# Optimization experiments

Hardware: AMD Instinct MI355X
Metric: run time of the kernel (lower is better)

## Reference

```python
import jax, jax.numpy as jnp
import numpy as np

B, S, D, H, L = 128, 200, 512, 512, 2  # batch, seq(=max_seq_len), input, hidden, layers


def _uni(key, shape, fan):
    bound = 1.0 / np.sqrt(fan)
    return jax.random.uniform(key, shape, jnp.float32, -bound, bound)


def setup_inputs() -> dict:
    key = jax.random.key(0)
    ks = jax.random.split(key, 12)
    x = jax.random.normal(ks[0], (B, S, D), jnp.float32)
    lens = jax.random.randint(ks[1], (B,), 1, S + 1).astype(jnp.int64)
    return {
        'x': x,
        'lens': lens,
        'Wih_f': _uni(ks[2], (L, 4 * H, D), H),
        'Whh_f': _uni(ks[3], (L, 4 * H, H), H),
        'bih_f': _uni(ks[4], (L, 4 * H), H),
        'bhh_f': _uni(ks[5], (L, 4 * H), H),
        'Wih_b': _uni(ks[6], (L, 4 * H, D), H),
        'Whh_b': _uni(ks[7], (L, 4 * H, H), H),
        'bih_b': _uni(ks[8], (L, 4 * H), H),
        'bhh_b': _uni(ks[9], (L, 4 * H), H),
    }


def _lstm_dir(xs, Wih, Whh, bih, bhh, reverse):
    # xs: [B,S,Din]. Precompute batched input projection, scan the recurrence.
    gx = jnp.einsum('bsd,gd->bsg', xs, Wih) + bih  # [B,S,4H]
    h0 = jnp.zeros((xs.shape[0], Whh.shape[1]), xs.dtype)
    c0 = jnp.zeros_like(h0)

    def step(carry, g_t):
        h, c = carry
        gates = g_t + h @ Whh.T + bhh
        i, f, g, o = jnp.split(gates, 4, axis=-1)  # PyTorch LSTMCell order
        i = jax.nn.sigmoid(i)
        f = jax.nn.sigmoid(f)
        g = jnp.tanh(g)
        o = jax.nn.sigmoid(o)
        c = f * c + i * g
        h = o * jnp.tanh(c)
        return (h, c), h

    _, hs = jax.lax.scan(step, (h0, c0), jnp.swapaxes(gx, 0, 1), reverse=reverse)
    return jnp.swapaxes(hs, 0, 1)  # [B,S,H], time-ordered


def reference(x, lens, Wih_f, Whh_f, bih_f, bhh_f, Wih_b, Whh_b, bih_b, bhh_b):
    valid = (jnp.arange(S)[None, :] < lens[:, None]).astype(x.dtype)[..., None]  # [B,S,1]
    f_in, b_in = x, x
    for l in range(L):
        f_h = _lstm_dir(f_in, Wih_f[l], Whh_f[l], bih_f[l], bhh_f[l], reverse=False)
        b_h = _lstm_dir(b_in, Wih_b[l], Whh_b[l], bih_b[l], bhh_b[l], reverse=True)
        f_h = f_h * valid  # masked_fill(mask, 0) for positions >= lens
        b_h = b_h * valid
        f_in, b_in = f_h, b_h
    return jnp.concatenate((f_in, b_in), axis=2)  # [B,S,2H]
```

## Files before the change

kernel.cpp:

```cpp
#include <hip/hip_runtime.h>
#include <hip/hip_bf16.h>

typedef __bf16 bf16x8 __attribute__((ext_vector_type(8)));
typedef _Float16 f16x8 __attribute__((ext_vector_type(8)));
typedef float f32x4 __attribute__((ext_vector_type(4)));

__device__ __forceinline__ unsigned short f2bf(float f) {
    unsigned int u = __builtin_bit_cast(unsigned int, f);
    u += 0x7FFFu + ((u >> 16) & 1u);
    return (unsigned short)(u >> 16);
}
__device__ __forceinline__ float bf2f(unsigned short s) {
    unsigned int u = ((unsigned int)s) << 16;
    return __builtin_bit_cast(float, u);
}

__device__ __forceinline__ void ldg_c(uint4& d, const void* p) {
    asm volatile("global_load_dwordx4 %0, %1, off sc0 sc1" : "=v"(d) : "v"(p));
}
__device__ __forceinline__ void vm_drain() {
    asm volatile("s_waitcnt vmcnt(0)" ::: "memory");
    __builtin_amdgcn_sched_barrier(0);
}
__device__ __forceinline__ void lds_fence() {
    asm volatile("s_waitcnt lgkmcnt(0)" ::: "memory");
    __builtin_amdgcn_sched_barrier(0);
}
__device__ __forceinline__ void stg_c16(void* p, unsigned short v) {
    asm volatile("global_store_short %0, %1, off sc0 sc1" :: "v"(p), "v"(v) : "memory");
}

__device__ __forceinline__ void wait_flags(const unsigned* f, unsigned tgt) {
    int lane = threadIdx.x & 63;
    for (;;) {
        unsigned v = __hip_atomic_load(f + lane, __ATOMIC_RELAXED, __HIP_MEMORY_SCOPE_AGENT);
        if (__all((int)(v >= tgt))) break;
        __builtin_amdgcn_s_sleep(1);
    }
}

__global__ void prep_x(const float* __restrict__ x,
                       unsigned short* __restrict__ xh,
                       unsigned short* __restrict__ xl) {
    int g = blockIdx.x * 256 + threadIdx.x;
    if (g >= 1638400) return;
    int lane = g & 63;
    int kc   = (g >> 6) & 15;
    int nt   = (g >> 10) & 7;
    int t    = g >> 13;
    int batch = nt * 16 + (lane & 15);
    int k = kc * 32 + (lane >> 4) * 8;
    const float* s = x + ((size_t)batch * 200 + t) * 512 + k;
    float4 v0 = *(const float4*)s;
    float4 v1 = *(const float4*)(s + 4);
    float vv[8] = {v0.x, v0.y, v0.z, v0.w, v1.x, v1.y, v1.z, v1.w};
    unsigned int ph[4], pl[4];
    #pragma unroll
    for (int j = 0; j < 4; ++j) {
        float a = vv[2*j], b = vv[2*j+1];
        unsigned short ha = f2bf(a), hb = f2bf(b);
        unsigned short la = f2bf(a - bf2f(ha)), lb = f2bf(b - bf2f(hb));
        ph[j] = (unsigned)ha | ((unsigned)hb << 16);
        pl[j] = (unsigned)la | ((unsigned)lb << 16);
    }
    ((uint4*)xh)[g] = make_uint4(ph[0], ph[1], ph[2], ph[3]);
    ((uint4*)xl)[g] = make_uint4(pl[0], pl[1], pl[2], pl[3]);
}

__global__ void prep_w(const float* __restrict__ W,
                       unsigned short* __restrict__ wprep,
                       int dir, int isHH) {
    int g = blockIdx.x * 256 + threadIdx.x;
    if (g >= 262144) return;
    int lane = g & 63;
    int kc   = (g >> 6) & 15;
    int mt   = (g >> 10) & 1;
    int cu   = (g >> 11) & 63;
    int l    = g >> 17;
    int r = lane & 15;
    int grow = (2 * mt + (r >> 3)) * 512 + cu * 8 + (r & 7);
    int k = kc * 32 + (lane >> 4) * 8;
    const float* s = W + ((size_t)l * 2048 + grow) * 512 + k;
    float4 v0 = *(const float4*)s;
    float4 v1 = *(const float4*)(s + 4);
    float vv[8] = {v0.x, v0.y, v0.z, v0.w, v1.x, v1.y, v1.z, v1.w};
    bool f16fmt = isHH || (l == 1);
    unsigned int ph[4], pl[4];
    #pragma unroll
    for (int j = 0; j < 4; ++j) {
        float a = vv[2*j], b = vv[2*j+1];
        unsigned short ha, hb, la, lb;
        if (f16fmt) {
            _Float16 fa = (_Float16)a, fb = (_Float16)b;
            _Float16 ra = (_Float16)(a - (float)fa), rb = (_Float16)(b - (float)fb);
            ha = __builtin_bit_cast(unsigned short, fa);
            hb = __builtin_bit_cast(unsigned short, fb);
            la = __builtin_bit_cast(unsigned short, ra);
            lb = __builtin_bit_cast(unsigned short, rb);
        } else {
            ha = f2bf(a); hb = f2bf(b);
            la = f2bf(a - bf2f(ha)); lb = f2bf(b - bf2f(hb));
        }
        ph[j] = (unsigned)ha | ((unsigned)hb << 16);
        pl[j] = (unsigned)la | ((unsigned)lb << 16);
    }
    size_t blk = ((size_t)(dir * 2 + l) * 64 + cu) * 8192;
    size_t fH = blk + (size_t)((isHH * 2 + 0) * 2048 + mt * 1024 + kc * 64 + lane);
    size_t fL = blk + (size_t)((isHH * 2 + 1) * 2048 + mt * 1024 + kc * 64 + lane);
    ((uint4*)wprep)[fH] = make_uint4(ph[0], ph[1], ph[2], ph[3]);
    ((uint4*)wprep)[fL] = make_uint4(pl[0], pl[1], pl[2], pl[3]);
}

__global__ void bsum_k(const float* __restrict__ bih_f, const float* __restrict__ bhh_f,
                       const float* __restrict__ bih_b, const float* __restrict__ bhh_b,
                       float* __restrict__ bsum) {
    int i = blockIdx.x * 256 + threadIdx.x;
    if (i < 8192) {
        int dir = i >> 12, rem = i & 4095;
        const float* bi = dir ? bih_b : bih_f;
        const float* bh = dir ? bhh_b : bhh_f;
        bsum[i] = bi[rem] + bh[rem];
    }
}

__global__ void reset_k(uint4* __restrict__ p) {
    int g = blockIdx.x * 256 + threadIdx.x;
    if (g < 131136) p[g] = make_uint4(0, 0, 0, 0);
}

__global__ void __launch_bounds__(512)
lstm_persist(const unsigned short* __restrict__ xh,
             const unsigned short* __restrict__ xl,
             const unsigned short* __restrict__ wprep,
             const float*          __restrict__ bsum,
             unsigned short*       __restrict__ hbuf,
             const int*            __restrict__ lens,
             float*                __restrict__ dout,
             unsigned*             __restrict__ flagv)
{
    extern __shared__ char smem[];
    float* wexch = (float*)(smem + 131072);
    float* cst   = (float*)(smem + 131072 + 17408);

    const int bid  = blockIdx.x;
    const int xcd  = bid & 7;
    const int unit = xcd >> 1;
    const int slot = unit >> 1, dir = unit & 1;
    const int cu8  = ((xcd & 1) << 5) | (bid >> 3);
    const int hj0  = cu8 * 8;
    const int tid  = threadIdx.x;
    const int lane = tid & 63, ng = tid >> 6;
    const int l15  = lane & 15, kg = lane >> 4;
    const int wsel = dir * 2 + slot;

    const int sib = slot ? dir : (2 + dir);
    unsigned* own_f = flagv + unit * 64;
    unsigned* sib_f = flagv + sib * 64;

    {
        const uint4* src = (const uint4*)wprep + ((size_t)(wsel * 64 + cu8) * 8192);
        uint4* dst = (uint4*)smem;
        #pragma unroll
        for (int i = 0; i < 16; ++i) dst[tid + i * 512] = src[tid + i * 512];
    }
    for (int i = tid; i < 8 * 132; i += 512) cst[i] = 0.f;
    __syncthreads();

    const int lenv = lens[ng * 16 + l15];
    const int u    = lane >> 3;
    const int b2   = 2 * (lane & 7);
    const int gbA  = ng * 16 + b2, gbB = gbA + 1;
    const int lenA = lens[gbA], lenB = lens[gbB];
    const int hj   = hj0 + u;
    float bias_c[4];
    #pragma unroll
    for (int q = 0; q < 4; ++q) bias_c[q] = bsum[wsel * 2048 + q * 512 + hj];
    float* wex = wexch + ng * 32 * 17;
    const size_t lofs = (size_t)lane * 8;

    for (int tau = 0; tau <= 200; ++tau) {
        const int t = slot ? (tau - 1) : tau;
        const bool active = (t >= 0 && t <= 199);
        int t_eff = 0, p_w = 0, p_r = 0;
        if (active) { t_eff = dir ? (199 - t) : t; p_w = t & 3; p_r = (t + 3) & 3; }

        f32x4 acc0 = {0.f, 0.f, 0.f, 0.f};
        f32x4 acc1 = {0.f, 0.f, 0.f, 0.f};

        if (slot == 0 && active) {
            const unsigned short* XH = xh + (size_t)t_eff * 65536;
            const unsigned short* XL = xl + (size_t)t_eff * 65536;
            #pragma unroll
            for (int kc = 0; kc < 16; ++kc) {
                size_t bo = (size_t)ng * 8192 + (size_t)kc * 512 + lofs;
                bf16x8 bxh = *(const bf16x8*)(XH + bo);
                bf16x8 bxl = *(const bf16x8*)(XL + bo);
                const char* ab = smem + kc * 1024 + lane * 16;
                bf16x8 aih0 = *(const bf16x8*)(ab);
                bf16x8 ail0 = *(const bf16x8*)(ab + 32768);
                bf16x8 aih1 = *(const bf16x8*)(ab + 16384);
                bf16x8 ail1 = *(const bf16x8*)(ab + 16384 + 32768);
                acc0 = __builtin_amdgcn_mfma_f32_16x16x32_bf16(aih0, bxh, acc0, 0, 0, 0);
                acc0 = __builtin_amdgcn_mfma_f32_16x16x32_bf16(aih0, bxl, acc0, 0, 0, 0);
                acc0 = __builtin_amdgcn_mfma_f32_16x16x32_bf16(ail0, bxh, acc0, 0, 0, 0);
                acc1 = __builtin_amdgcn_mfma_f32_16x16x32_bf16(aih1, bxh, acc1, 0, 0, 0);
                acc1 = __builtin_amdgcn_mfma_f32_16x16x32_bf16(aih1, bxl, acc1, 0, 0, 0);
                acc1 = __builtin_amdgcn_mfma_f32_16x16x32_bf16(ail1, bxh, acc1, 0, 0, 0);
            }
        }

        {
            unsigned tgt = (unsigned)tau;
            if (ng == 0) wait_flags(own_f, tgt);
            if (slot == 1) { if (ng == 1) wait_flags(sib_f, tgt); }
            else if (tau >= 3) { if (ng == 1) wait_flags(sib_f, tgt - 2); }
        }
        __syncthreads();

        if (active) {
            const unsigned short* HH = hbuf + ((size_t)((slot * 4 + p_r) * 2 + dir) << 16);

            if (slot == 0) {
                uint4 vh[16];
                #pragma unroll
                for (int kc = 0; kc < 16; ++kc)
                    ldg_c(vh[kc], HH + (size_t)ng * 8192 + (size_t)kc * 512 + lofs);
                vm_drain();
                #pragma unroll
                for (int kc = 0; kc < 16; ++kc) {
                    f16x8 bh = __builtin_bit_cast(f16x8, vh[kc]);
                    const char* ab = smem + kc * 1024 + lane * 16;
                    f16x8 ahh0 = *(const f16x8*)(ab + 65536);
                    f16x8 ahl0 = *(const f16x8*)(ab + 98304);
                    f16x8 ahh1 = *(const f16x8*)(ab + 16384 + 65536);
                    f16x8 ahl1 = *(const f16x8*)(ab + 16384 + 98304);
                    acc0 = __builtin_amdgcn_mfma_f32_16x16x32_f16(ahh0, bh, acc0, 0, 0, 0);
                    acc0 = __builtin_amdgcn_mfma_f32_16x16x32_f16(ahl0, bh, acc0, 0, 0, 0);
                    acc1 = __builtin_amdgcn_mfma_f32_16x16x32_f16(ahh1, bh, acc1, 0, 0, 0);
                    acc1 = __builtin_amdgcn_mfma_f32_16x16x32_f16(ahl1, bh, acc1, 0, 0, 0);
                }
            } else {
                int p_x = t & 3;
                const unsigned short* XHc = hbuf + ((size_t)(p_x * 2 + dir) << 16);
                uint4 vx[16], vh[16];
                #pragma unroll
                for (int kc = 0; kc < 16; ++kc) {
                    size_t bo = (size_t)ng * 8192 + (size_t)kc * 512 + lofs;
                    ldg_c(vx[kc], XHc + bo);
                    ldg_c(vh[kc], HH + bo);
                }
                vm_drain();
                const bool mv = (t_eff < lenv);
                #pragma unroll
                for (int kc = 0; kc < 16; ++kc) {
                    if (!mv) vx[kc] = make_uint4(0, 0, 0, 0);
                    f16x8 xv = __builtin_bit_cast(f16x8, vx[kc]);
                    f16x8 bh = __builtin_bit_cast(f16x8, vh[kc]);
                    const char* ab = smem + kc * 1024 + lane * 16;
                    f16x8 aih0 = *(const f16x8*)(ab);
                    f16x8 ail0 = *(const f16x8*)(ab + 32768);
                    f16x8 ahh0 = *(const f16x8*)(ab + 65536);
                    f16x8 ahl0 = *(const f16x8*)(ab + 98304);
                    f16x8 aih1 = *(const f16x8*)(ab + 16384);
                    f16x8 ail1 = *(const f16x8*)(ab + 16384 + 32768);
                    f16x8 ahh1 = *(const f16x8*)(ab + 16384 + 65536);
                    f16x8 ahl1 = *(const f16x8*)(ab + 16384 + 98304);
                    acc0 = __builtin_amdgcn_mfma_f32_16x16x32_f16(aih0, xv, acc0, 0, 0, 0);
                    acc0 = __builtin_amdgcn_mfma_f32_16x16x32_f16(ail0, xv, acc0, 0, 0, 0);
                    acc0 = __builtin_amdgcn_mfma_f32_16x16x32_f16(ahh0, bh, acc0, 0, 0, 0);
                    acc0 = __builtin_amdgcn_mfma_f32_16x16x32_f16(ahl0, bh, acc0, 0, 0, 0);
                    acc1 = __builtin_amdgcn_mfma_f32_16x16x32_f16(aih1, xv, acc1, 0, 0, 0);
                    acc1 = __builtin_amdgcn_mfma_f32_16x16x32_f16(ail1, xv, acc1, 0, 0, 0);
                    acc1 = __builtin_amdgcn_mfma_f32_16x16x32_f16(ahh1, bh, acc1, 0, 0, 0);
                    acc1 = __builtin_amdgcn_mfma_f32_16x16x32_f16(ahl1, bh, acc1, 0, 0, 0);
                }
            }

            #pragma unroll
            for (int r = 0; r < 4; ++r) {
                wex[(kg * 4 + r) * 17 + l15]        = acc0[r];
                wex[(16 + kg * 4 + r) * 17 + l15]   = acc1[r];
            }
            lds_fence();

            unsigned short* Hw = hbuf + ((size_t)((slot * 4 + p_w) * 2 + dir) << 16);
            #pragma unroll
            for (int j = 0; j < 2; ++j) {
                int b  = b2 + j;
                int gb = ng * 16 + b;
                float g0 = wex[(0 * 8 + u) * 17 + b] + bias_c[0];
                float g1 = wex[(1 * 8 + u) * 17 + b] + bias_c[1];
                float g2 = wex[(2 * 8 + u) * 17 + b] + bias_c[2];
                float g3 = wex[(3 * 8 + u) * 17 + b] + bias_c[3];
                float cv = cst[u * 132 + gb];
                float iG = 1.f / (1.f + expf(-g0));
                float fG = 1.f / (1.f + expf(-g1));
                float gG = tanhf(g2);
                float oG = 1.f / (1.f + expf(-g3));
                float cn = fG * cv + iG * gG;
                cst[u * 132 + gb] = cn;
                float hn = oG * tanhf(cn);
                _Float16 hf = (_Float16)hn;
                size_t ho = (((size_t)ng * 16 + (hj >> 5)) * 64
                             + ((hj >> 3) & 3) * 16 + b) * 8 + (hj & 7);
                stg_c16(Hw + ho, __builtin_bit_cast(unsigned short, hf));
                if (slot) {
                    float hm = (t_eff < (j ? lenB : lenA)) ? hn : 0.f;
                    dout[((size_t)gb * 200 + t_eff) * 1024 + dir * 512 + hj] = hm;
                }
            }
            vm_drain();
        }

        __syncthreads();
        if (tid == 0)
            __hip_atomic_store(own_f + cu8, (unsigned)(tau + 1),
                               __ATOMIC_RELAXED, __HIP_MEMORY_SCOPE_AGENT);
    }
}

extern "C" void kernel_launch(void* const* d_in, const int* in_sizes, int n_in,
                              void* d_out, int out_size, void* d_ws, size_t ws_size,
                              hipStream_t stream) {
    const float* x     = (const float*)d_in[0];
    const int*   lens  = (const int*)d_in[1];
    const float* Wih_f = (const float*)d_in[2];
    const float* Whh_f = (const float*)d_in[3];
    const float* bih_f = (const float*)d_in[4];
    const float* bhh_f = (const float*)d_in[5];
    const float* Wih_b = (const float*)d_in[6];
    const float* Whh_b = (const float*)d_in[7];
    const float* bih_b = (const float*)d_in[8];
    const float* bhh_b = (const float*)d_in[9];
    float* out = (float*)d_out;
    char* ws = (char*)d_ws;
    if (ws_size < 88114176) return;

    unsigned short* xh    = (unsigned short*)(ws);
    unsigned short* xl    = (unsigned short*)(ws + 26214400);
    unsigned short* wprep = (unsigned short*)(ws + 52428800);
    float*          bsum  = (float*)(ws + 85983232);
    unsigned short* hbuf  = (unsigned short*)(ws + 86016000);
    unsigned*       flg   = (unsigned*)(ws + 88113152);

    prep_x<<<6400, 256, 0, stream>>>(x, xh, xl);
    prep_w<<<1024, 256, 0, stream>>>(Wih_f, wprep, 0, 0);
    prep_w<<<1024, 256, 0, stream>>>(Whh_f, wprep, 0, 1);
    prep_w<<<1024, 256, 0, stream>>>(Wih_b, wprep, 1, 0);
    prep_w<<<1024, 256, 0, stream>>>(Whh_b, wprep, 1, 1);
    bsum_k<<<32, 256, 0, stream>>>(bih_f, bhh_f, bih_b, bhh_b, bsum);
    reset_k<<<513, 256, 0, stream>>>((uint4*)hbuf);

    static const int LDS_BYTES = 131072 + 17408 + 4224;
    hipFuncSetAttribute(reinterpret_cast<const void*>(lstm_persist),
                        hipFuncAttributeMaxDynamicSharedMemorySize, LDS_BYTES);

    void* args[] = {(void*)&xh, (void*)&xl, (void*)&wprep, (void*)&bsum,
                    (void*)&hbuf, (void*)&lens, (void*)&out, (void*)&flg};
    hipLaunchCooperativeKernel(reinterpret_cast<void*>(lstm_persist),
                               dim3(256), dim3(512), args, LDS_BYTES, stream);
}
```

Measured before the change: 1.772 ms.

## Pipeline h-state loads with staged waitcnt, pack h stores, prefetch flag probe

Global loads of the recurrent h vector (and, for layer 2, the layer-1 input) are now consumed in groups of four with partial vmcnt waits, so MFMAs start before all loads land. Layer-2 issues the h loads first so the recurrent part can start early, then does the input projection. The gate/cell epilogue is remapped so each lane handles two adjacent hidden units of one batch row. This allows packed 32-bit h stores and float2 output stores in place of scattered 16-bit and 32-bit stores. A flag probe is issued before the x-projection to skip the spin loop when the dependency is already met, and biases move to LDS.

```diff
diff --git a/kernel.cpp b/kernel.cpp
--- a/kernel.cpp
+++ b/kernel.cpp
@@ -18,16 +18,29 @@
 __device__ __forceinline__ void ldg_c(uint4& d, const void* p) {
     asm volatile("global_load_dwordx4 %0, %1, off sc0 sc1" : "=v"(d) : "v"(p));
 }
+__device__ __forceinline__ void stg_c32(void* p, unsigned v) {
+    asm volatile("global_store_dword %0, %1, off sc0 sc1" :: "v"(p), "v"(v) : "memory");
+}
 __device__ __forceinline__ void vm_drain() {
     asm volatile("s_waitcnt vmcnt(0)" ::: "memory");
     __builtin_amdgcn_sched_barrier(0);
 }
+__device__ __forceinline__ void vm_wait_imm(int n) {
+    switch (n) {
+    case 0:  asm volatile("s_waitcnt vmcnt(0)"  ::: "memory"); break;
+    case 4:  asm volatile("s_waitcnt vmcnt(4)"  ::: "memory"); break;
+    case 8:  asm volatile("s_waitcnt vmcnt(8)"  ::: "memory"); break;
+    case 12: asm volatile("s_waitcnt vmcnt(12)" ::: "memory"); break;
+    case 16: asm volatile("s_waitcnt vmcnt(16)" ::: "memory"); break;
+    case 20: asm volatile("s_waitcnt vmcnt(20)" ::: "memory"); break;
+    case 24: asm volatile("s_waitcnt vmcnt(24)" ::: "memory"); break;
+    default: asm volatile("s_waitcnt vmcnt(28)" ::: "memory"); break;
+    }
+    __builtin_amdgcn_sched_barrier(0);
+}
 __device__ __forceinline__ void lds_fence() {
     asm volatile("s_waitcnt lgkmcnt(0)" ::: "memory");
     __builtin_amdgcn_sched_barrier(0);
-}
-__device__ __forceinline__ void stg_c16(void* p, unsigned short v) {
-    asm volatile("global_store_short %0, %1, off sc0 sc1" :: "v"(p), "v"(v) : "memory");
 }
 
 __device__ __forceinline__ void wait_flags(const unsigned* f, unsigned tgt) {
@@ -139,8 +152,9 @@
              unsigned*             __restrict__ flagv)
 {
     extern __shared__ char smem[];
-    float* wexch = (float*)(smem + 131072);
-    float* cst   = (float*)(smem + 131072 + 17408);
+    float* wexch  = (float*)(smem + 131072);
+    float* cst    = (float*)(smem + 131072 + 17408);
+    float* bias_l = (float*)(smem + 131072 + 17408 + 4224);
 
     const int bid  = blockIdx.x;
     const int xcd  = bid & 7;
@@ -164,19 +178,15 @@
         for (int i = 0; i < 16; ++i) dst[tid + i * 512] = src[tid + i * 512];
     }
     for (int i = tid; i < 8 * 132; i += 512) cst[i] = 0.f;
+    if (tid < 32) bias_l[tid] = bsum[wsel * 2048 + (tid >> 3) * 512 + hj0 + (tid & 7)];
     __syncthreads();
 
     const int lenv = lens[ng * 16 + l15];
-    const int u    = lane >> 3;
-    const int b2   = 2 * (lane & 7);
-    const int gbA  = ng * 16 + b2, gbB = gbA + 1;
-    const int lenA = lens[gbA], lenB = lens[gbB];
-    const int hj   = hj0 + u;
-    float bias_c[4];
-    #pragma unroll
-    for (int q = 0; q < 4; ++q) bias_c[q] = bsum[wsel * 2048 + q * 512 + hj];
+    const int gb   = ng * 16 + l15;
+    const int u0   = kg * 2;
+    const size_t lofs = (size_t)lane * 8;
+    const size_t hoff = ((size_t)(ng * 16 + (cu8 >> 2)) * 64 + (cu8 & 3) * 16 + l15) * 8 + u0;
     float* wex = wexch + ng * 32 * 17;
-    const size_t lofs = (size_t)lane * 8;
 
     for (int tau = 0; tau <= 200; ++tau) {
         const int t = slot ? (tau - 1) : tau;
@@ -186,6 +196,10 @@
 
         f32x4 acc0 = {0.f, 0.f, 0.f, 0.f};
         f32x4 acc1 = {0.f, 0.f, 0.f, 0.f};
+
+        unsigned probe = 0u;
+        if (slot == 0 && ng == 0)
+            probe = __hip_atomic_load(own_f + lane, __ATOMIC_RELAXED, __HIP_MEMORY_SCOPE_AGENT);
 
         if (slot == 0 && active) {
             const unsigned short* XH = xh + (size_t)t_eff * 65536;
@@ -209,11 +223,13 @@
             }
         }
 
-        {
-            unsigned tgt = (unsigned)tau;
-            if (ng == 0) wait_flags(own_f, tgt);
-            if (slot == 1) { if (ng == 1) wait_flags(sib_f, tgt); }
-            else if (tau >= 3) { if (ng == 1) wait_flags(sib_f, tgt - 2); }
+        if (slot == 0) {
+            if (ng == 0 && !__all((int)(probe >= (unsigned)tau)))
+                wait_flags(own_f, (unsigned)tau);
+            if (ng == 1 && tau >= 3) wait_flags(sib_f, (unsigned)(tau - 2));
+        } else {
+            if (ng == 0) wait_flags(own_f, (unsigned)tau);
+            if (ng == 1) wait_flags(sib_f, (unsigned)tau);
         }
         __syncthreads();
 
@@ -225,73 +241,87 @@
                 #pragma unroll
                 for (int kc = 0; kc < 16; ++kc)
                     ldg_c(vh[kc], HH + (size_t)ng * 8192 + (size_t)kc * 512 + lofs);
-                vm_drain();
-                #pragma unroll
-                for (int kc = 0; kc < 16; ++kc) {
-                    f16x8 bh = __builtin_bit_cast(f16x8, vh[kc]);
-                    const char* ab = smem + kc * 1024 + lane * 16;
-                    f16x8 ahh0 = *(const f16x8*)(ab + 65536);
-                    f16x8 ahl0 = *(const f16x8*)(ab + 98304);
-                    f16x8 ahh1 = *(const f16x8*)(ab + 16384 + 65536);
-                    f16x8 ahl1 = *(const f16x8*)(ab + 16384 + 98304);
-                    acc0 = __builtin_amdgcn_mfma_f32_16x16x32_f16(ahh0, bh, acc0, 0, 0, 0);
-                    acc0 = __builtin_amdgcn_mfma_f32_16x16x32_f16(ahl0, bh, acc0, 0, 0, 0);
-                    acc1 = __builtin_amdgcn_mfma_f32_16x16x32_f16(ahh1, bh, acc1, 0, 0, 0);
-                    acc1 = __builtin_amdgcn_mfma_f32_16x16x32_f16(ahl1, bh, acc1, 0, 0, 0);
+                #pragma unroll
+                for (int g = 0; g < 4; ++g) {
+                    vm_wait_imm(12 - 4 * g);
+                    #pragma unroll
+                    for (int k2 = 0; k2 < 4; ++k2) {
+                        int kc = g * 4 + k2;
+                        f16x8 bh = __builtin_bit_cast(f16x8, vh[kc]);
+                        const char* ab = smem + kc * 1024 + lane * 16;
+                        f16x8 ahh0 = *(const f16x8*)(ab + 65536);
+                        f16x8 ahl0 = *(const f16x8*)(ab + 98304);
+                        f16x8 ahh1 = *(const f16x8*)(ab + 16384 + 65536);
+                        f16x8 ahl1 = *(const f16x8*)(ab + 16384 + 98304);
+                        acc0 = __builtin_amdgcn_mfma_f32_16x16x32_f16(ahh0, bh, acc0, 0, 0, 0);
+                        acc0 = __builtin_amdgcn_mfma_f32_16x16x32_f16(ahl0, bh, acc0, 0, 0, 0);
+                        acc1 = __builtin_amdgcn_mfma_f32_16x16x32_f16(ahh1, bh, acc1, 0, 0, 0);
+                        acc1 = __builtin_amdgcn_mfma_f32_16x16x32_f16(ahl1, bh, acc1, 0, 0, 0);
+                    }
                 }
             } else {
                 int p_x = t & 3;
                 const unsigned short* XHc = hbuf + ((size_t)(p_x * 2 + dir) << 16);
-                uint4 vx[16], vh[16];
-                #pragma unroll
-                for (int kc = 0; kc < 16; ++kc) {
-                    size_t bo = (size_t)ng * 8192 + (size_t)kc * 512 + lofs;
-                    ldg_c(vx[kc], XHc + bo);
-                    ldg_c(vh[kc], HH + bo);
+                uint4 vh[16], vx[16];
+                #pragma unroll
+                for (int kc = 0; kc < 16; ++kc)
+                    ldg_c(vh[kc], HH + (size_t)ng * 8192 + (size_t)kc * 512 + lofs);
+                #pragma unroll
+                for (int kc = 0; kc < 16; ++kc)
+                    ldg_c(vx[kc], XHc + (size_t)ng * 8192 + (size_t)kc * 512 + lofs);
+                #pragma unroll
+                for (int g = 0; g < 4; ++g) {
+                    vm_wait_imm(28 - 4 * g);
+                    #pragma unroll
+                    for (int k2 = 0; k2 < 4; ++k2) {
+                        int kc = g * 4 + k2;
+                        f16x8 bh = __builtin_bit_cast(f16x8, vh[kc]);
+                        const char* ab = smem + kc * 1024 + lane * 16;
+                        f16x8 ahh0 = *(const f16x8*)(ab + 65536);
+                        f16x8 ahl0 = *(const f16x8*)(ab + 98304);
+                        f16x8 ahh1 = *(const f16x8*)(ab + 16384 + 65536);
+                        f16x8 ahl1 = *(const f16x8*)(ab + 16384 + 98304);
+                        acc0 = __builtin_amdgcn_mfma_f32_16x16x32_f16(ahh0, bh, acc0, 0, 0, 0);
+                        acc0 = __builtin_amdgcn_mfma_f32_16x16x32_f16(ahl0, bh, acc0, 0, 0, 0);
+                        acc1 = __builtin_amdgcn_mfma_f32_16x16x32_f16(ahh1, bh, acc1, 0, 0, 0);
+                        acc1 = __builtin_amdgcn_mfma_f32_16x16x32_f16(ahl1, bh, acc1, 0, 0, 0);
+                    }
                 }
-                vm_drain();
                 const bool mv = (t_eff < lenv);
                 #pragma unroll
-                for (int kc = 0; kc < 16; ++kc) {
-                    if (!mv) vx[kc] = make_uint4(0, 0, 0, 0);
-                    f16x8 xv = __builtin_bit_cast(f16x8, vx[kc]);
-                    f16x8 bh = __builtin_bit_cast(f16x8, vh[kc]);
-                    const char* ab = smem + kc * 1024 + lane * 16;
-                    f16x8 aih0 = *(const f16x8*)(ab);
-                    f16x8 ail0 = *(const f16x8*)(ab + 32768);
-                    f16x8 ahh0 = *(const f16x8*)(ab + 65536);
-                    f16x8 ahl0 = *(const f16x8*)(ab + 98304);
-                    f16x8 aih1 = *(const f16x8*)(ab + 16384);
-                    f16x8 ail1 = *(const f16x8*)(ab + 16384 + 32768);
-                    f16x8 ahh1 = *(const f16x8*)(ab + 16384 + 65536);
-                    f16x8 ahl1 = *(const f16x8*)(ab + 16384 + 98304);
-                    acc0 = __builtin_amdgcn_mfma_f32_16x16x32_f16(aih0, xv, acc0, 0, 0, 0);
-                    acc0 = __builtin_amdgcn_mfma_f32_16x16x32_f16(ail0, xv, acc0, 0, 0, 0);
-                    acc0 = __builtin_amdgcn_mfma_f32_16x16x32_f16(ahh0, bh, acc0, 0, 0, 0);
-                    acc0 = __builtin_amdgcn_mfma_f32_16x16x32_f16(ahl0, bh, acc0, 0, 0, 0);
-                    acc1 = __builtin_amdgcn_mfma_f32_16x16x32_f16(aih1, xv, acc1, 0, 0, 0);
-                    acc1 = __builtin_amdgcn_mfma_f32_16x16x32_f16(ail1, xv, acc1, 0, 0, 0);
-                    acc1 = __builtin_amdgcn_mfma_f32_16x16x32_f16(ahh1, bh, acc1, 0, 0, 0);
-                    acc1 = __builtin_amdgcn_mfma_f32_16x16x32_f16(ahl1, bh, acc1, 0, 0, 0);
+                for (int g = 0; g < 4; ++g) {
+                    vm_wait_imm(12 - 4 * g);
+                    #pragma unroll
+                    for (int k2 = 0; k2 < 4; ++k2) {
+                        int kc = g * 4 + k2;
+                        if (!mv) vx[kc] = make_uint4(0, 0, 0, 0);
+                        f16x8 xv = __builtin_bit_cast(f16x8, vx[kc]);
+                        const char* ab = smem + kc * 1024 + lane * 16;
+                        f16x8 aih0 = *(const f16x8*)(ab);
+                        f16x8 aih1 = *(const f16x8*)(ab + 16384);
+                        acc0 = __builtin_amdgcn_mfma_f32_16x16x32_f16(aih0, xv, acc0, 0, 0, 0);
+                        acc1 = __builtin_amdgcn_mfma_f32_16x16x32_f16(aih1, xv, acc1, 0, 0, 0);
+                    }
                 }
             }
 
             #pragma unroll
             for (int r = 0; r < 4; ++r) {
-                wex[(kg * 4 + r) * 17 + l15]        = acc0[r];
-                wex[(16 + kg * 4 + r) * 17 + l15]   = acc1[r];
+                wex[(kg * 4 + r) * 17 + l15]      = acc0[r];
+                wex[(16 + kg * 4 + r) * 17 + l15] = acc1[r];
             }
             lds_fence();
 
             unsigned short* Hw = hbuf + ((size_t)((slot * 4 + p_w) * 2 + dir) << 16);
+            unsigned hpk = 0;
+            float hm0 = 0.f, hm1 = 0.f;
             #pragma unroll
             for (int j = 0; j < 2; ++j) {
-                int b  = b2 + j;
-                int gb = ng * 16 + b;
-                float g0 = wex[(0 * 8 + u) * 17 + b] + bias_c[0];
-                float g1 = wex[(1 * 8 + u) * 17 + b] + bias_c[1];
-                float g2 = wex[(2 * 8 + u) * 17 + b] + bias_c[2];
-                float g3 = wex[(3 * 8 + u) * 17 + b] + bias_c[3];
+                int u = u0 + j;
+                float g0 = wex[(0  + u) * 17 + l15] + bias_l[u];
+                float g1 = wex[(8  + u) * 17 + l15] + bias_l[8 + u];
+                float g2 = wex[(16 + u) * 17 + l15] + bias_l[16 + u];
+                float g3 = wex[(24 + u) * 17 + l15] + bias_l[24 + u];
                 float cv = cst[u * 132 + gb];
                 float iG = 1.f / (1.f + expf(-g0));
                 float fG = 1.f / (1.f + expf(-g1));
@@ -301,13 +331,14 @@
                 cst[u * 132 + gb] = cn;
                 float hn = oG * tanhf(cn);
                 _Float16 hf = (_Float16)hn;
-                size_t ho = (((size_t)ng * 16 + (hj >> 5)) * 64
-                             + ((hj >> 3) & 3) * 16 + b) * 8 + (hj & 7);
-                stg_c16(Hw + ho, __builtin_bit_cast(unsigned short, hf));
-                if (slot) {
-                    float hm = (t_eff < (j ? lenB : lenA)) ? hn : 0.f;
-                    dout[((size_t)gb * 200 + t_eff) * 1024 + dir * 512 + hj] = hm;
-                }
+                hpk |= ((unsigned)__builtin_bit_cast(unsigned short, hf)) << (16 * j);
+                float hm = (t_eff < lenv) ? hn : 0.f;
+                if (j) hm1 = hm; else hm0 = hm;
+            }
+            stg_c32(Hw + hoff, hpk);
+            if (slot) {
+                float2 o = make_float2(hm0, hm1);
+                *(float2*)(dout + ((size_t)gb * 200 + t_eff) * 1024 + dir * 512 + hj0 + u0) = o;
             }
             vm_drain();
         }
@@ -351,7 +382,7 @@
     bsum_k<<<32, 256, 0, stream>>>(bih_f, bhh_f, bih_b, bhh_b, bsum);
     reset_k<<<513, 256, 0, stream>>>((uint4*)hbuf);
 
-    static const int LDS_BYTES = 131072 + 17408 + 4224;
+    static const int LDS_BYTES = 131072 + 17408 + 4224 + 128;
     hipFuncSetAttribute(reinterpret_cast<const void*>(lstm_persist),
                         hipFuncAttributeMaxDynamicSharedMemorySize, LDS_BYTES);
 
```

New measurement: 1.837 ms. 3.7% more time.
